# Kernel optimization log

Measured on AMD Instinct MI355X. Metric: run time of the kernel, lower is better.

## Reference

```python
import jax, jax.numpy as jnp
import numpy as np
import math

HIDDEN = 1024
NUM_LAYERS = 24
INIT_RANGE = 0.02


def setup_inputs() -> dict:
    key = jax.random.key(0)
    k1, k2 = jax.random.split(key)
    B, S, H = 4, 4096, HIDDEN
    hidden_states = jax.random.normal(k1, (B, S, H), dtype=jnp.float32)
    std = INIT_RANGE / math.sqrt(2.0 * NUM_LAYERS * H)
    # queries weight: [H, H], applied as F.linear => x @ W^T
    W_q = jax.random.normal(k2, (H, H), dtype=jnp.float32) * std
    return {"hidden_states": hidden_states, "W_q": W_q}


def reference(hidden_states, W_q):
    # queries = F.linear(x, W) = x @ W^T          [B, S, H]
    q = jnp.einsum('bsh,oh->bso', hidden_states, W_q)
    # pre_attn = Q @ K^T where K = x             [B, S, S]
    pre_attn = jnp.einsum('bso,bto->bst', q, hidden_states)
    # attention = pre_attn @ V where V = x       [B, S, H]
    attention = jnp.einsum('bst,bth->bsh', pre_attn, hidden_states)
    return attention
```

## Files before the change

kernel.cpp:

```cpp
#include <hip/hip_runtime.h>
#include <hip/hip_bf16.h>
#include <stdint.h>

#define H_DIM 1024
#define S_DIM 4096
#define B_DIM 4

typedef __bf16 bf16x8 __attribute__((ext_vector_type(8)));
typedef float f32x4 __attribute__((ext_vector_type(4)));
typedef unsigned short u16x4 __attribute__((ext_vector_type(4)));
typedef unsigned short u16x8 __attribute__((ext_vector_type(8)));

__device__ __forceinline__ unsigned short f2bf(float f) {
    union { float f; uint32_t u; } v; v.f = f;
    uint32_t u = v.u;
    uint32_t r = (u + 0x7FFFu + ((u >> 16) & 1u)) >> 16;
    return (unsigned short)r;
}
__device__ __forceinline__ float bf2f(unsigned short u) {
    union { uint32_t u; float f; } v; v.u = (uint32_t)u << 16; return v.f;
}

__device__ __forceinline__ void gate_vmcnt4() {
    __builtin_amdgcn_sched_barrier(0);
    asm volatile("s_waitcnt vmcnt(4)");
    __builtin_amdgcn_sched_barrier(0);
}
__device__ __forceinline__ void gate_vmcnt0() {
    __builtin_amdgcn_sched_barrier(0);
    asm volatile("s_waitcnt vmcnt(0)");
    __builtin_amdgcn_sched_barrier(0);
}
__device__ __forceinline__ void gate_lgkm0() {
    asm volatile("s_waitcnt lgkmcnt(0)");
    __builtin_amdgcn_sched_barrier(0);
}

template <int IMM>
__device__ __forceinline__ bf16x8 ds_read_b128_imm(unsigned addr) {
    bf16x8 r;
    asm volatile("ds_read_b128 %0, %1 offset:%2"
                 : "=v"(r) : "v"(addr), "i"(IMM));
    return r;
}

__global__ __launch_bounds__(256)
void cast_x_kernel(const float* __restrict__ X,
                   unsigned short* __restrict__ Xb,
                   unsigned short* __restrict__ XT) {
    __shared__ float tile[64][65];
    const int b  = blockIdx.z;
    const int h0 = blockIdx.x * 64;
    const int s0 = blockIdx.y * 64;
    const int tx = threadIdx.x;
    const int ty = threadIdx.y;
#pragma unroll
    for (int j = 0; j < 4; ++j) {
        int s = ty + 16 * j;
        f32x4 v = *(const f32x4*)&X[((size_t)b * S_DIM + s0 + s) * H_DIM + h0 + tx * 4];
        u16x4 o;
#pragma unroll
        for (int k = 0; k < 4; ++k) {
            tile[s][tx * 4 + k] = v[k];
            o[k] = f2bf(v[k]);
        }
        *(u16x4*)&Xb[((size_t)b * S_DIM + s0 + s) * H_DIM + h0 + tx * 4] = o;
    }
    __syncthreads();
#pragma unroll
    for (int j = 0; j < 4; ++j) {
        int hh = ty + 16 * j;
        u16x4 o;
#pragma unroll
        for (int k = 0; k < 4; ++k)
            o[k] = f2bf(tile[tx * 4 + k][hh]);
        *(u16x4*)&XT[((size_t)b * H_DIM + h0 + hh) * S_DIM + s0 + tx * 4] = o;
    }
}

__global__ void cast_w_kernel(const float* __restrict__ W,
                              unsigned short* __restrict__ WT) {
    __shared__ float tile[32][33];
    const int b0 = blockIdx.x * 32;
    const int o0 = blockIdx.y * 32;
    const int tx = threadIdx.x;
    const int ty = threadIdx.y;
#pragma unroll
    for (int i = 0; i < 4; ++i) {
        int o = ty + 8 * i;
        tile[o][tx] = W[(size_t)(o0 + o) * H_DIM + b0 + tx];
    }
    __syncthreads();
#pragma unroll
    for (int i = 0; i < 4; ++i) {
        int bb = ty + 8 * i;
        WT[(size_t)(b0 + bb) * H_DIM + o0 + tx] = f2bf(tile[tx][bb]);
    }
}

template <int NSPLIT>
__global__ void reduce_cast_u16_kernel(const unsigned short* __restrict__ P,
                                       unsigned short* __restrict__ Out,
                                       size_t sSplit) {
    size_t i = ((size_t)blockIdx.x * blockDim.x + threadIdx.x) * 8;
    float s[8] = {0.f, 0.f, 0.f, 0.f, 0.f, 0.f, 0.f, 0.f};
#pragma unroll
    for (int sp = 0; sp < NSPLIT; ++sp) {
        u16x8 u = *(const u16x8*)&P[(size_t)sp * sSplit + i];
#pragma unroll
        for (int k = 0; k < 8; ++k) s[k] += bf2f(u[k]);
    }
    u16x8 o;
#pragma unroll
    for (int k = 0; k < 8; ++k) o[k] = f2bf(s[k]);
    *(u16x8*)&Out[i] = o;
}

template <typename OutT, int NSPLIT>
__global__ __launch_bounds__(512, 2)
void gemm_c8_kernel(const unsigned short* __restrict__ A,
                    const unsigned short* __restrict__ Bt,
                    OutT* __restrict__ C,
                    int K, int lda, int ldb, int ldc,
                    size_t sA, size_t sB, size_t sC, size_t sSplit) {
    extern __shared__ char smem_raw[];

    const int tid  = threadIdx.x;
    const int w    = tid >> 6;
    const int lane = tid & 63;
    const int wm   = w & 1;
    const int wn   = w >> 1;
    const int q    = lane >> 4;
    const int col  = lane & 15;

    const int tileM = blockIdx.x * 256;
    const int tileN = blockIdx.y * 256;
    const int bz   = blockIdx.z / NSPLIT;
    const int sp   = blockIdx.z % NSPLIT;
    const int Ksub = K / NSPLIT;
    const int T    = Ksub >> 6;

    const unsigned short* Ab = A + sA * bz + (size_t)sp * Ksub;
    const unsigned short* Bb = Bt + sB * bz + (size_t)sp * Ksub;

    auto lds3 = (__attribute__((address_space(3))) char*)&smem_raw[0];
    const unsigned ldsBase = (unsigned)(size_t)lds3;

    const int slot = q ^ ((col >> 1) & 3);
    const unsigned aBase = ldsBase + (unsigned)(wm * 8192 + col * 64 + slot * 16);
    const unsigned bBase = ldsBase + 32768u + (unsigned)(wn * 4096 + col * 64 + slot * 16);

    const int lrow = lane >> 2;
    const int koff = ((lane & 3) ^ ((lane >> 3) & 3)) * 8;
    const unsigned short* pA[2];
    const unsigned short* pB[2];
    unsigned dstR[2];
#pragma unroll
    for (int j = 0; j < 2; ++j) {
        int g = 2 * w + j;
        pA[j] = Ab + (size_t)(tileM + g * 16 + lrow) * lda + koff;
        pB[j] = Bb + (size_t)(tileN + g * 16 + lrow) * ldb + koff;
        dstR[j] = (unsigned)(g * 1024);
    }
    auto stageA = [&](int tgt, int h) {
#pragma unroll
        for (int j = 0; j < 2; ++j)
            __builtin_amdgcn_global_load_lds(
                (const __attribute__((address_space(1))) void*)(pA[j] + tgt * 64 + h * 32),
                (__attribute__((address_space(3))) void*)(lds3 + ((unsigned)(tgt & 1) * 65536u + (unsigned)h * 16384u + dstR[j])),
                16, 0, 0);
    };
    auto stageB = [&](int tgt, int h) {
#pragma unroll
        for (int j = 0; j < 2; ++j)
            __builtin_amdgcn_global_load_lds(
                (const __attribute__((address_space(1))) void*)(pB[j] + tgt * 64 + h * 32),
                (__attribute__((address_space(3))) void*)(lds3 + ((unsigned)(tgt & 1) * 65536u + 32768u + (unsigned)h * 16384u + dstR[j])),
                16, 0, 0);
    };

    f32x4 acc[8][4];
#pragma unroll
    for (int r = 0; r < 8; ++r)
#pragma unroll
        for (int c = 0; c < 4; ++c)
            acc[r][c] = (f32x4){0.f, 0.f, 0.f, 0.f};

    stageA(0, 0); stageB(0, 0); stageA(0, 1); stageB(0, 1);

    for (int n = 0; n < T; ++n) {
        const unsigned aAddr = aBase + (unsigned)((n & 1) << 16);
        const unsigned bAddr = bBase + (unsigned)((n & 1) << 16);
        const bool pf = (n + 1 < T);
        bf16x8 av[4], bv[4];

        gate_vmcnt4();
        __builtin_amdgcn_s_barrier();

        av[0] = ds_read_b128_imm<0>(aAddr);
        av[1] = ds_read_b128_imm<1024>(aAddr);
        av[2] = ds_read_b128_imm<2048>(aAddr);
        av[3] = ds_read_b128_imm<3072>(aAddr);
        bv[0] = ds_read_b128_imm<0>(bAddr);
        bv[1] = ds_read_b128_imm<1024>(bAddr);
        bv[2] = ds_read_b128_imm<2048>(bAddr);
        bv[3] = ds_read_b128_imm<3072>(bAddr);
        if (pf) stageA(n + 1, 0);
        gate_lgkm0();
        __builtin_amdgcn_s_setprio(1);
#pragma unroll
        for (int mf = 0; mf < 4; ++mf)
#pragma unroll
            for (int nf = 0; nf < 4; ++nf)
                acc[mf][nf] = __builtin_amdgcn_mfma_f32_16x16x32_bf16(
                    av[mf], bv[nf], acc[mf][nf], 0, 0, 0);
        __builtin_amdgcn_s_setprio(0);

        av[0] = ds_read_b128_imm<4096>(aAddr);
        av[1] = ds_read_b128_imm<5120>(aAddr);
        av[2] = ds_read_b128_imm<6144>(aAddr);
        av[3] = ds_read_b128_imm<7168>(aAddr);
        if (pf) stageB(n + 1, 0);
        gate_lgkm0();
        __builtin_amdgcn_s_setprio(1);
#pragma unroll
        for (int mf = 0; mf < 4; ++mf)
#pragma unroll
            for (int nf = 0; nf < 4; ++nf)
                acc[4 + mf][nf] = __builtin_amdgcn_mfma_f32_16x16x32_bf16(
                    av[mf], bv[nf], acc[4 + mf][nf], 0, 0, 0);
        __builtin_amdgcn_s_setprio(0);

        if (pf) gate_vmcnt4();
        else    gate_vmcnt0();
        __builtin_amdgcn_s_barrier();

        av[0] = ds_read_b128_imm<16384 + 0>(aAddr);
        av[1] = ds_read_b128_imm<16384 + 1024>(aAddr);
        av[2] = ds_read_b128_imm<16384 + 2048>(aAddr);
        av[3] = ds_read_b128_imm<16384 + 3072>(aAddr);
        bv[0] = ds_read_b128_imm<16384 + 0>(bAddr);
        bv[1] = ds_read_b128_imm<16384 + 1024>(bAddr);
        bv[2] = ds_read_b128_imm<16384 + 2048>(bAddr);
        bv[3] = ds_read_b128_imm<16384 + 3072>(bAddr);
        if (pf) stageA(n + 1, 1);
        gate_lgkm0();
        __builtin_amdgcn_s_setprio(1);
#pragma unroll
        for (int mf = 0; mf < 4; ++mf)
#pragma unroll
            for (int nf = 0; nf < 4; ++nf)
                acc[mf][nf] = __builtin_amdgcn_mfma_f32_16x16x32_bf16(
                    av[mf], bv[nf], acc[mf][nf], 0, 0, 0);
        __builtin_amdgcn_s_setprio(0);

        av[0] = ds_read_b128_imm<16384 + 4096>(aAddr);
        av[1] = ds_read_b128_imm<16384 + 5120>(aAddr);
        av[2] = ds_read_b128_imm<16384 + 6144>(aAddr);
        av[3] = ds_read_b128_imm<16384 + 7168>(aAddr);
        if (pf) stageB(n + 1, 1);
        gate_lgkm0();
        __builtin_amdgcn_s_setprio(1);
#pragma unroll
        for (int mf = 0; mf < 4; ++mf)
#pragma unroll
            for (int nf = 0; nf < 4; ++nf)
                acc[4 + mf][nf] = __builtin_amdgcn_mfma_f32_16x16x32_bf16(
                    av[mf], bv[nf], acc[4 + mf][nf], 0, 0, 0);
        __builtin_amdgcn_s_setprio(0);
    }

    OutT* Cb = C + sC * bz + sSplit * sp;
    __syncthreads();
    float* lws = (float*)(smem_raw) + (size_t)w * 1088;
    const int lr = lane >> 4;
    const int lc = lane & 15;
#pragma unroll
    for (int mf = 0; mf < 8; ++mf) {
#pragma unroll
        for (int nf = 0; nf < 4; ++nf)
#pragma unroll
            for (int v = 0; v < 4; ++v)
                lws[(q * 4 + v) * 68 + nf * 16 + col] = acc[mf][nf][v];
#pragma unroll
        for (int p = 0; p < 4; ++p) {
            f32x4 t = *(const f32x4*)&lws[(p * 4 + lr) * 68 + lc * 4];
            int row  = tileM + wm * 128 + mf * 16 + p * 4 + lr;
            int colg = tileN + wn * 64 + lc * 4;
            if constexpr (sizeof(OutT) == 2) {
                u16x4 u;
                u[0] = f2bf(t[0]); u[1] = f2bf(t[1]);
                u[2] = f2bf(t[2]); u[3] = f2bf(t[3]);
                *(u16x4*)&Cb[(size_t)row * ldc + colg] = u;
            } else {
                *(f32x4*)&Cb[(size_t)row * ldc + colg] = t;
            }
        }
    }
}

extern "C" void kernel_launch(void* const* d_in, const int* in_sizes, int n_in,
                              void* d_out, int out_size, void* d_ws, size_t ws_size,
                              hipStream_t stream) {
    const float* X = (const float*)d_in[0];
    const float* W = (const float*)d_in[1];
    float* out = (float*)d_out;

    char* ws = (char*)d_ws;
    unsigned short* Xb = (unsigned short*)(ws);
    unsigned short* XT = (unsigned short*)(ws + 33554432);
    unsigned short* WT = (unsigned short*)(ws + 67108864);
    unsigned short* G  = (unsigned short*)(ws + 69206016);
    unsigned short* MT = (unsigned short*)(ws + 77594624);
    unsigned short* Gpart  = (unsigned short*)(ws + 85983232);
    unsigned short* MTpart = (unsigned short*)(ws + 85983232);

    const size_t sBH = (size_t)B_DIM * H_DIM * H_DIM;

    cast_x_kernel<<<dim3(H_DIM / 64, S_DIM / 64, B_DIM), dim3(16, 16), 0, stream>>>(X, Xb, XT);
    cast_w_kernel<<<dim3(H_DIM / 32, H_DIM / 32, 1), dim3(32, 8), 0, stream>>>(W, WT);

    gemm_c8_kernel<unsigned short, 4><<<dim3(4, 4, B_DIM * 4), 512, 131072, stream>>>(
        XT, XT, Gpart, S_DIM, S_DIM, S_DIM, H_DIM,
        (size_t)H_DIM * S_DIM, (size_t)H_DIM * S_DIM, (size_t)H_DIM * H_DIM, sBH);
    reduce_cast_u16_kernel<4><<<dim3(sBH / 8 / 256), 256, 0, stream>>>(Gpart, G, sBH);

    gemm_c8_kernel<unsigned short, 4><<<dim3(4, 4, B_DIM * 4), 512, 131072, stream>>>(
        G, WT, MTpart, H_DIM, H_DIM, H_DIM, H_DIM,
        (size_t)H_DIM * H_DIM, (size_t)0, (size_t)H_DIM * H_DIM, sBH);
    reduce_cast_u16_kernel<4><<<dim3(sBH / 8 / 256), 256, 0, stream>>>(MTpart, MT, sBH);

    gemm_c8_kernel<float, 1><<<dim3(S_DIM / 256, H_DIM / 256, B_DIM), 512, 131072, stream>>>(
        Xb, MT, out, H_DIM, H_DIM, H_DIM, H_DIM,
        (size_t)S_DIM * H_DIM, (size_t)H_DIM * H_DIM, (size_t)S_DIM * H_DIM, 0);
}
```

Measured before the change: 228.0 us.

## Fuse all stages into one cooperative persistent kernel with grid syncs

Replaces the seven separate launches (casts, three split-K GEMMs, two reductions) with a single cooperative kernel of 256 blocks that runs each stage in turn, separated by grid-wide syncs. It is meant to remove per-launch overhead and the gaps between kernels. In exchange, every stage is limited to 256 blocks of 512 threads, so the cast and reduce stages lose parallelism, and each grid sync adds barrier cost. It also depends on the cooperative launch fitting 256 resident blocks with 128KB of LDS each.

Measured after the change: 620.1 us. 172% more time.

```diff
diff --git a/kernel.cpp b/kernel.cpp
--- a/kernel.cpp
+++ b/kernel.cpp
@@ -1,6 +1,9 @@
 #include <hip/hip_runtime.h>
+#include <hip/hip_cooperative_groups.h>
 #include <hip/hip_bf16.h>
 #include <stdint.h>
+
+namespace cg = cooperative_groups;
 
 #define H_DIM 1024
 #define S_DIM 4096
@@ -44,85 +47,14 @@
     return r;
 }
 
-__global__ __launch_bounds__(256)
-void cast_x_kernel(const float* __restrict__ X,
-                   unsigned short* __restrict__ Xb,
-                   unsigned short* __restrict__ XT) {
-    __shared__ float tile[64][65];
-    const int b  = blockIdx.z;
-    const int h0 = blockIdx.x * 64;
-    const int s0 = blockIdx.y * 64;
-    const int tx = threadIdx.x;
-    const int ty = threadIdx.y;
-#pragma unroll
-    for (int j = 0; j < 4; ++j) {
-        int s = ty + 16 * j;
-        f32x4 v = *(const f32x4*)&X[((size_t)b * S_DIM + s0 + s) * H_DIM + h0 + tx * 4];
-        u16x4 o;
-#pragma unroll
-        for (int k = 0; k < 4; ++k) {
-            tile[s][tx * 4 + k] = v[k];
-            o[k] = f2bf(v[k]);
-        }
-        *(u16x4*)&Xb[((size_t)b * S_DIM + s0 + s) * H_DIM + h0 + tx * 4] = o;
-    }
-    __syncthreads();
-#pragma unroll
-    for (int j = 0; j < 4; ++j) {
-        int hh = ty + 16 * j;
-        u16x4 o;
-#pragma unroll
-        for (int k = 0; k < 4; ++k)
-            o[k] = f2bf(tile[tx * 4 + k][hh]);
-        *(u16x4*)&XT[((size_t)b * H_DIM + h0 + hh) * S_DIM + s0 + tx * 4] = o;
-    }
-}
-
-__global__ void cast_w_kernel(const float* __restrict__ W,
-                              unsigned short* __restrict__ WT) {
-    __shared__ float tile[32][33];
-    const int b0 = blockIdx.x * 32;
-    const int o0 = blockIdx.y * 32;
-    const int tx = threadIdx.x;
-    const int ty = threadIdx.y;
-#pragma unroll
-    for (int i = 0; i < 4; ++i) {
-        int o = ty + 8 * i;
-        tile[o][tx] = W[(size_t)(o0 + o) * H_DIM + b0 + tx];
-    }
-    __syncthreads();
-#pragma unroll
-    for (int i = 0; i < 4; ++i) {
-        int bb = ty + 8 * i;
-        WT[(size_t)(b0 + bb) * H_DIM + o0 + tx] = f2bf(tile[tx][bb]);
-    }
-}
-
-template <int NSPLIT>
-__global__ void reduce_cast_u16_kernel(const unsigned short* __restrict__ P,
-                                       unsigned short* __restrict__ Out,
-                                       size_t sSplit) {
-    size_t i = ((size_t)blockIdx.x * blockDim.x + threadIdx.x) * 8;
-    float s[8] = {0.f, 0.f, 0.f, 0.f, 0.f, 0.f, 0.f, 0.f};
-#pragma unroll
-    for (int sp = 0; sp < NSPLIT; ++sp) {
-        u16x8 u = *(const u16x8*)&P[(size_t)sp * sSplit + i];
-#pragma unroll
-        for (int k = 0; k < 8; ++k) s[k] += bf2f(u[k]);
-    }
-    u16x8 o;
-#pragma unroll
-    for (int k = 0; k < 8; ++k) o[k] = f2bf(s[k]);
-    *(u16x8*)&Out[i] = o;
-}
-
 template <typename OutT, int NSPLIT>
-__global__ __launch_bounds__(512, 2)
-void gemm_c8_kernel(const unsigned short* __restrict__ A,
-                    const unsigned short* __restrict__ Bt,
-                    OutT* __restrict__ C,
-                    int K, int lda, int ldb, int ldc,
-                    size_t sA, size_t sB, size_t sC, size_t sSplit) {
+__device__ __forceinline__ void gemm_body(
+    const unsigned short* __restrict__ A,
+    const unsigned short* __restrict__ Bt,
+    OutT* __restrict__ C,
+    int K, int lda, int ldb, int ldc,
+    size_t sA, size_t sB, size_t sC, size_t sSplit,
+    int bx, int by, int bz_raw) {
     extern __shared__ char smem_raw[];
 
     const int tid  = threadIdx.x;
@@ -133,10 +65,10 @@
     const int q    = lane >> 4;
     const int col  = lane & 15;
 
-    const int tileM = blockIdx.x * 256;
-    const int tileN = blockIdx.y * 256;
-    const int bz   = blockIdx.z / NSPLIT;
-    const int sp   = blockIdx.z % NSPLIT;
+    const int tileM = bx * 256;
+    const int tileN = by * 256;
+    const int bz   = bz_raw / NSPLIT;
+    const int sp   = bz_raw % NSPLIT;
     const int Ksub = K / NSPLIT;
     const int T    = Ksub >> 6;
 
@@ -297,16 +229,72 @@
             }
         }
     }
-}
-
-extern "C" void kernel_launch(void* const* d_in, const int* in_sizes, int n_in,
-                              void* d_out, int out_size, void* d_ws, size_t ws_size,
-                              hipStream_t stream) {
-    const float* X = (const float*)d_in[0];
-    const float* W = (const float*)d_in[1];
-    float* out = (float*)d_out;
-
-    char* ws = (char*)d_ws;
+    __syncthreads();
+}
+
+template <int NSPLIT>
+__device__ __forceinline__ void reduce_body(const unsigned short* __restrict__ P,
+                                            unsigned short* __restrict__ Out,
+                                            size_t sSplit, int bid, int tid) {
+#pragma unroll
+    for (int it = 0; it < 4; ++it) {
+        size_t i = ((size_t)(it * 131072 + bid * 512 + tid)) * 8;
+        float s[8] = {0.f, 0.f, 0.f, 0.f, 0.f, 0.f, 0.f, 0.f};
+#pragma unroll
+        for (int sp = 0; sp < NSPLIT; ++sp) {
+            u16x8 u = *(const u16x8*)&P[(size_t)sp * sSplit + i];
+#pragma unroll
+            for (int k = 0; k < 8; ++k) s[k] += bf2f(u[k]);
+        }
+        u16x8 o;
+#pragma unroll
+        for (int k = 0; k < 8; ++k) o[k] = f2bf(s[k]);
+        *(u16x8*)&Out[i] = o;
+    }
+}
+
+template <bool DUAL>
+__device__ __forceinline__ void cast_tile(const float* __restrict__ src, int lds_,
+                                          unsigned short* __restrict__ dstN,
+                                          unsigned short* __restrict__ dstT, int ldt,
+                                          int tid) {
+    extern __shared__ char smem_raw[];
+    float* tile = (float*)smem_raw;
+    const int tx = tid & 15;
+    const int ty = tid >> 4;
+#pragma unroll
+    for (int jj = 0; jj < 2; ++jj) {
+        int s = ty + 32 * jj;
+        f32x4 v = *(const f32x4*)&src[(size_t)s * lds_ + tx * 4];
+        u16x4 o;
+#pragma unroll
+        for (int k = 0; k < 4; ++k) {
+            tile[s * 65 + tx * 4 + k] = v[k];
+            o[k] = f2bf(v[k]);
+        }
+        if constexpr (DUAL)
+            *(u16x4*)&dstN[(size_t)s * lds_ + tx * 4] = o;
+    }
+    __syncthreads();
+#pragma unroll
+    for (int jj = 0; jj < 2; ++jj) {
+        int hh = ty + 32 * jj;
+        u16x4 o;
+#pragma unroll
+        for (int k = 0; k < 4; ++k)
+            o[k] = f2bf(tile[(tx * 4 + k) * 65 + hh]);
+        *(u16x4*)&dstT[(size_t)hh * ldt + tx * 4] = o;
+    }
+    __syncthreads();
+}
+
+__global__ __launch_bounds__(512, 2)
+void mega_kernel(const float* __restrict__ X, const float* __restrict__ W,
+                 float* __restrict__ out, char* __restrict__ ws) {
+    cg::grid_group grid = cg::this_grid();
+    const int bid = blockIdx.x;
+    const int tid = threadIdx.x;
+
     unsigned short* Xb = (unsigned short*)(ws);
     unsigned short* XT = (unsigned short*)(ws + 33554432);
     unsigned short* WT = (unsigned short*)(ws + 67108864);
@@ -314,23 +302,63 @@
     unsigned short* MT = (unsigned short*)(ws + 77594624);
     unsigned short* Gpart  = (unsigned short*)(ws + 85983232);
     unsigned short* MTpart = (unsigned short*)(ws + 85983232);
-
     const size_t sBH = (size_t)B_DIM * H_DIM * H_DIM;
 
-    cast_x_kernel<<<dim3(H_DIM / 64, S_DIM / 64, B_DIM), dim3(16, 16), 0, stream>>>(X, Xb, XT);
-    cast_w_kernel<<<dim3(H_DIM / 32, H_DIM / 32, 1), dim3(32, 8), 0, stream>>>(W, WT);
-
-    gemm_c8_kernel<unsigned short, 4><<<dim3(4, 4, B_DIM * 4), 512, 131072, stream>>>(
-        XT, XT, Gpart, S_DIM, S_DIM, S_DIM, H_DIM,
-        (size_t)H_DIM * S_DIM, (size_t)H_DIM * S_DIM, (size_t)H_DIM * H_DIM, sBH);
-    reduce_cast_u16_kernel<4><<<dim3(sBH / 8 / 256), 256, 0, stream>>>(Gpart, G, sBH);
-
-    gemm_c8_kernel<unsigned short, 4><<<dim3(4, 4, B_DIM * 4), 512, 131072, stream>>>(
-        G, WT, MTpart, H_DIM, H_DIM, H_DIM, H_DIM,
-        (size_t)H_DIM * H_DIM, (size_t)0, (size_t)H_DIM * H_DIM, sBH);
-    reduce_cast_u16_kernel<4><<<dim3(sBH / 8 / 256), 256, 0, stream>>>(MTpart, MT, sBH);
-
-    gemm_c8_kernel<float, 1><<<dim3(S_DIM / 256, H_DIM / 256, B_DIM), 512, 131072, stream>>>(
-        Xb, MT, out, H_DIM, H_DIM, H_DIM, H_DIM,
-        (size_t)S_DIM * H_DIM, (size_t)H_DIM * H_DIM, (size_t)S_DIM * H_DIM, 0);
-}
+    {
+        const int o0 = (bid & 15) * 64, b0 = (bid >> 4) * 64;
+        cast_tile<false>(W + (size_t)o0 * H_DIM + b0, H_DIM,
+                         nullptr,
+                         WT + (size_t)b0 * H_DIM + o0, H_DIM, tid);
+        for (int i = 0; i < 16; ++i) {
+            int t = bid * 16 + i;
+            int b = t >> 10;
+            int rem = t & 1023;
+            int h0 = (rem & 15) * 64, s0 = (rem >> 4) * 64;
+            cast_tile<true>(X + ((size_t)b * S_DIM + s0) * H_DIM + h0, H_DIM,
+                            Xb + ((size_t)b * S_DIM + s0) * H_DIM + h0,
+                            XT + ((size_t)b * H_DIM + h0) * S_DIM + s0, S_DIM, tid);
+        }
+    }
+    __threadfence();
+    grid.sync();
+
+    gemm_body<unsigned short, 4>(XT, XT, Gpart,
+        S_DIM, S_DIM, S_DIM, H_DIM,
+        (size_t)H_DIM * S_DIM, (size_t)H_DIM * S_DIM, (size_t)H_DIM * H_DIM, sBH,
+        bid & 3, (bid >> 2) & 3, bid >> 4);
+    __threadfence();
+    grid.sync();
+
+    reduce_body<4>(Gpart, G, sBH, bid, tid);
+    __threadfence();
+    grid.sync();
+
+    gemm_body<unsigned short, 4>(G, WT, MTpart,
+        H_DIM, H_DIM, H_DIM, H_DIM,
+        (size_t)H_DIM * H_DIM, (size_t)0, (size_t)H_DIM * H_DIM, sBH,
+        bid & 3, (bid >> 2) & 3, bid >> 4);
+    __threadfence();
+    grid.sync();
+
+    reduce_body<4>(MTpart, MT, sBH, bid, tid);
+    __threadfence();
+    grid.sync();
+
+    gemm_body<float, 1>(Xb, MT, out,
+        H_DIM, H_DIM, H_DIM, H_DIM,
+        (size_t)S_DIM * H_DIM, (size_t)H_DIM * H_DIM, (size_t)S_DIM * H_DIM, 0,
+        bid & 15, (bid >> 4) & 3, bid >> 6);
+}
+
+extern "C" void kernel_launch(void* const* d_in, const int* in_sizes, int n_in,
+                              void* d_out, int out_size, void* d_ws, size_t ws_size,
+                              hipStream_t stream) {
+    const float* X = (const float*)d_in[0];
+    const float* W = (const float*)d_in[1];
+    float* out = (float*)d_out;
+    char* ws = (char*)d_ws;
+
+    void* args[] = {(void*)&X, (void*)&W, (void*)&out, (void*)&ws};
+    (void)hipLaunchCooperativeKernel((const void*)mega_kernel,
+                                     dim3(256), dim3(512), args, 131072, stream);
+}
```
